# Kernel tuning notes

Hardware: AMD Instinct MI355X
Metric: run time of the kernel (lower is better)

The kernel has to match this reference:

```python
import jax, jax.numpy as jnp
import numpy as np

TAU = 1.0  # temperaturesa
GRID = 5   # torch.chunk(..., 5) along H and W


def _cam(X, gamma, tau):
    # Channel attention: energy = Xf Xf^T over spatial dim, with max-subtraction/negation trick.
    B, C, H, W = X.shape
    Xf = X.reshape(B, C, H * W)
    energy = jnp.einsum('bcn,bdn->bcd', Xf, Xf)                      # [B,C,C]
    energy_new = jnp.max(energy, axis=-1, keepdims=True) - energy
    attn = jax.nn.softmax(energy_new / tau, axis=-1)
    out = jnp.einsum('bcd,bdn->bcn', attn, Xf).reshape(B, C, H, W)
    return gamma * out + X


def _pam(X, Wq, bq, Wk, bk, Wv, bv, gamma, tau):
    # Position attention with 1x1-conv q/k/v (1x1 conv == channel matmul).
    B, C, H, W = X.shape
    N = H * W
    Xf = X.reshape(B, C, N)
    q = jnp.einsum('kc,bcn->bnk', Wq, Xf) + bq                        # [B,N,C//8]
    k = jnp.einsum('kc,bcn->bkn', Wk, Xf) + bk[None, :, None]         # [B,C//8,N]
    v = jnp.einsum('dc,bcn->bdn', Wv, Xf) + bv[None, :, None]         # [B,C,N]
    energy = jnp.einsum('bnk,bkm->bnm', q, k)                         # [B,N,N]
    attn = jax.nn.softmax(energy / tau, axis=-1)
    # torch: bmm(value, attention.permute(0,2,1)) -> out[b,d,m] = sum_n v[b,d,n]*attn[b,m,n]
    out = jnp.einsum('bdn,bmn->bdm', v, attn).reshape(B, C, H, W)
    return gamma * out + X


def _cka_loss(X, Y):
    # linear_CKA_loss: HKH centering done as K - rowmean - colmean + totalmean.
    def cgram(Z):
        K = Z @ Z.T                                                   # [B,B]
        rm = jnp.mean(K, axis=1, keepdims=True)
        cm = jnp.mean(K, axis=0, keepdims=True)
        return K - rm - cm + jnp.mean(K)
    cX, cY = cgram(X), cgram(Y)
    hsic = jnp.sum(cX * cY)
    v1 = jnp.sqrt(jnp.sum(cX * cX))
    v2 = jnp.sqrt(jnp.sum(cY * cY))
    return -jnp.log(jnp.abs(hsic / (v1 * v2)) + 1e-8)


def _grid_chunks(X, g=GRID):
    # 5x5 spatial tiling -> [g*g, B, C, H/g, W/g]
    B, C, H, W = X.shape
    h, w = H // g, W // g
    return X.reshape(B, C, g, h, g, w).transpose(2, 4, 0, 1, 3, 5).reshape(g * g, B, C, h, w)


def setup_inputs() -> dict:
    key = jax.random.key(0)
    ks = jax.random.split(key, 10)
    B, C, H, W = 16, 256, 80, 80
    Ck = C // 8
    return {
        'feat_S': jax.random.normal(ks[0], (B, C, H, W), jnp.float32),
        'feat_T': jax.random.normal(ks[1], (B, C, H, W), jnp.float32),
        'Wq': jax.random.normal(ks[2], (Ck, C), jnp.float32),
        'bq': jax.random.normal(ks[3], (Ck,), jnp.float32),
        'Wk': jax.random.normal(ks[4], (Ck, C), jnp.float32),
        'bk': jax.random.normal(ks[5], (Ck,), jnp.float32),
        'Wv': jax.random.normal(ks[6], (C, C), jnp.float32),
        'bv': jax.random.normal(ks[7], (C,), jnp.float32),
        'gammacam': jax.random.normal(ks[8], (1,), jnp.float32),
        'gammapam': jax.random.normal(ks[9], (1,), jnp.float32),
    }


def reference(feat_S, feat_T, Wq, bq, Wk, bk, Wv, bv, gammacam, gammapam):
    # feature_transform == 'separately_CAMgridPAM_CKA'
    tau = TAU
    pam = lambda X: _pam(X, Wq, bq, Wk, bk, Wv, bv, gammapam, tau)
    chunks_S = _grid_chunks(feat_S)                                   # [25,B,C,16,16]
    chunks_T = _grid_chunks(feat_T)
    pam_S = jax.vmap(pam)(chunks_S)
    pam_T = jax.vmap(pam)(chunks_T)
    nchunk, B = pam_S.shape[0], pam_S.shape[1]
    flat_S = pam_S.reshape(nchunk, B, -1)
    flat_T = pam_T.reshape(nchunk, B, -1)
    loss_PAM = jnp.mean(jax.vmap(_cka_loss)(flat_S, flat_T))          # sum/n == mean
    CAM_S = _cam(feat_S, gammacam, tau)
    CAM_T = _cam(feat_T, gammacam, tau)
    loss_CAM = _cka_loss(CAM_S.reshape(B, -1), CAM_T.reshape(B, -1))
    return (loss_CAM, loss_PAM)
```

## Files before the change

kernel.cpp:

```cpp
#include <hip/hip_runtime.h>


typedef short bf16x8 __attribute__((ext_vector_type(8)));
typedef float f32x4 __attribute__((ext_vector_type(4)));

constexpr int BB = 16;
constexpr int CH = 256;
constexpr int HW = 6400;
constexpr int IMW = 80;

__device__ __forceinline__ int lds_off(int row, int half, int k2) {
  return row * 128 + ((((half << 6)) | k2) ^ ((row & 7) << 4));
}

__device__ __forceinline__ bf16x8 frag_ld(const char* base, int row, int half, int lane) {
  int off = row * 128 + ((((half << 6)) | ((lane >> 4) << 4)) ^ ((lane & 7) << 4));
  return *(const bf16x8*)(base + off);
}

__device__ __forceinline__ void cvt2(float x, unsigned short& h, unsigned short& l) {
  unsigned u = __float_as_uint(x);
  h = (unsigned short)(u >> 16);
  float r = x - __uint_as_float(u & 0xffff0000u);
  l = (unsigned short)(__float_as_uint(r) >> 16);
}

__device__ __forceinline__ void cvt4(float4 v, ushort4& h, ushort4& l) {
  cvt2(v.x, h.x, l.x); cvt2(v.y, h.y, l.y);
  cvt2(v.z, h.z, l.z); cvt2(v.w, h.w, l.w);
}

__device__ __forceinline__ void cvt8(float4 v0, float4 v1, bf16x8& hi, bf16x8& lo) {
  unsigned short h, l;
  cvt2(v0.x, h, l); hi[0] = (short)h; lo[0] = (short)l;
  cvt2(v0.y, h, l); hi[1] = (short)h; lo[1] = (short)l;
  cvt2(v0.z, h, l); hi[2] = (short)h; lo[2] = (short)l;
  cvt2(v0.w, h, l); hi[3] = (short)h; lo[3] = (short)l;
  cvt2(v1.x, h, l); hi[4] = (short)h; lo[4] = (short)l;
  cvt2(v1.y, h, l); hi[5] = (short)h; lo[5] = (short)l;
  cvt2(v1.z, h, l); hi[6] = (short)h; lo[6] = (short)l;
  cvt2(v1.w, h, l); hi[7] = (short)h; lo[7] = (short)l;
}

__device__ __forceinline__ unsigned short bf_rnd(float x) {
  unsigned u = __float_as_uint(x);
  return (unsigned short)((u + 0x8000u) >> 16);
}

__global__ __launch_bounds__(512) void cam_energy_k(const float* __restrict__ fS,
                                                    const float* __restrict__ fT,
                                                    float* __restrict__ part) {
  const int kc = blockIdx.x, b = blockIdx.y, t = blockIdx.z;
  const float* X = (t ? fT : fS) + (size_t)b * CH * HW;
  __shared__ unsigned short lds[2 * 256 * 64];
  const int tid = threadIdx.x, lane = tid & 63, w = tid >> 6;
  const int wr = w >> 2, wc = w & 3;
  const int r0 = tid >> 1, half = tid & 1;
  const int kbase = kc * 800 + half * 32;
  const float* Xr = X + (size_t)r0 * HW + kbase;
  f32x4 acc[8][4] = {};
  float4 v[8];
#pragma unroll
  for (int q = 0; q < 8; ++q) v[q] = *(const float4*)(Xr + q * 4);
  for (int it = 0; it < 13; ++it) {
    char* pb = (char*)lds + (it & 1) * 32768;
#pragma unroll
    for (int q = 0; q < 8; ++q) {
      ushort4 u;
      u.x = bf_rnd(v[q].x); u.y = bf_rnd(v[q].y);
      u.z = bf_rnd(v[q].z); u.w = bf_rnd(v[q].w);
      *(ushort4*)(pb + lds_off(r0, half, q * 8)) = u;
    }
    __syncthreads();
    float4 nv[8];
    if (it < 12) {
      const int nk = (it + 1) * 64;
      if (nk + half * 32 < 800) {
        const float* Xn = Xr + nk;
#pragma unroll
        for (int q = 0; q < 8; ++q) nv[q] = *(const float4*)(Xn + q * 4);
      } else {
#pragma unroll
        for (int q = 0; q < 8; ++q) nv[q] = make_float4(0.f, 0.f, 0.f, 0.f);
      }
    }
    bf16x8 bfr[2][4];
#pragma unroll
    for (int h = 0; h < 2; ++h)
#pragma unroll
      for (int n = 0; n < 4; ++n)
        bfr[h][n] = frag_ld(pb, wc * 64 + n * 16 + (lane & 15), h, lane);
#pragma unroll
    for (int m = 0; m < 8; ++m) {
      int arow = wr * 128 + m * 16 + (lane & 15);
      bf16x8 a0 = frag_ld(pb, arow, 0, lane);
      bf16x8 a1 = frag_ld(pb, arow, 1, lane);
#pragma unroll
      for (int n = 0; n < 4; ++n)
        acc[m][n] = __builtin_amdgcn_mfma_f32_16x16x32_bf16(a0, bfr[0][n], acc[m][n], 0, 0, 0);
#pragma unroll
      for (int n = 0; n < 4; ++n)
        acc[m][n] = __builtin_amdgcn_mfma_f32_16x16x32_bf16(a1, bfr[1][n], acc[m][n], 0, 0, 0);
    }
#pragma unroll
    for (int q = 0; q < 8; ++q) v[q] = nv[q];
  }
  float* Eb = part + (((size_t)kc * 2 + t) * BB + b) * 65536;
#pragma unroll
  for (int m = 0; m < 8; ++m)
#pragma unroll
    for (int n = 0; n < 4; ++n) {
      int row = wr * 128 + m * 16 + ((lane >> 4) << 2);
      int col = wc * 64 + n * 16 + (lane & 15);
#pragma unroll
      for (int r2 = 0; r2 < 4; ++r2)
        Eb[(size_t)(row + r2) * 256 + col] = acc[m][n][r2];
    }
}

__global__ __launch_bounds__(64) void cam_softmax_k(float* __restrict__ part) {
  const int c = blockIdx.x, b = blockIdx.y, t = blockIdx.z;
  const size_t base = (((size_t)t * BB + b) * CH + c) * CH;
  const int lane = threadIdx.x;
  float4 x = make_float4(0.f, 0.f, 0.f, 0.f);
#pragma unroll
  for (int p = 0; p < 8; ++p) {
    float4 y = ((const float4*)(part + (size_t)p * 2097152 + base))[lane];
    x.x += y.x; x.y += y.y; x.z += y.z; x.w += y.w;
  }
  float mn = fminf(fminf(x.x, x.y), fminf(x.z, x.w));
  for (int o = 32; o; o >>= 1) mn = fminf(mn, __shfl_xor(mn, o));
  float4 p4;
  p4.x = __expf(mn - x.x); p4.y = __expf(mn - x.y);
  p4.z = __expf(mn - x.z); p4.w = __expf(mn - x.w);
  float s = (p4.x + p4.y) + (p4.z + p4.w);
  for (int o = 32; o; o >>= 1) s += __shfl_xor(s, o);
  const float inv = 1.0f / s;
  p4.x *= inv; p4.y *= inv; p4.z *= inv; p4.w *= inv;
  ((float4*)(part + base))[lane] = p4;
}

template <int MODE>
__global__ __launch_bounds__(512) void ax_k(const float* __restrict__ Abase, int Astride,
                                            const float* __restrict__ X,
                                            float* __restrict__ OUT,
                                            const float* __restrict__ bvec,
                                            const float* __restrict__ gsc) {
  const int nt = blockIdx.x;
  const int b = blockIdx.y;
  const float* A = Abase + (size_t)b * Astride;
  const float* Xb = X + (size_t)b * CH * HW;
  float* OUTb = OUT + (size_t)b * CH * HW;
  const int nbase = nt * 128;
  __shared__ unsigned short lds[(256 + 128) * 64];
  char* Ab = (char*)lds;
  char* Bb = (char*)lds + 32768;
  const int tid = threadIdx.x, lane = tid & 63, w = tid >> 6;
  const int wr = w >> 1, wc = w & 1;
  const int r0 = tid >> 1, kq = tid & 1;
  const int n4 = (tid & 31) * 4, c0l = tid >> 5;
  f32x4 acc[4][4] = {};
  float4 ra[4], rb[2];
#pragma unroll
  for (int q = 0; q < 4; ++q)
    ra[q] = *(const float4*)(A + (size_t)r0 * 256 + kq * 16 + q * 4);
#pragma unroll
  for (int q = 0; q < 2; ++q)
    rb[q] = *(const float4*)(Xb + (size_t)(c0l + 16 * q) * HW + nbase + n4);
  for (int s = 0; s < 8; ++s) {
#pragma unroll
    for (int q = 0; q < 4; ++q) {
      ushort4 h4, l4;
      cvt4(ra[q], h4, l4);
      *(ushort4*)(Ab + lds_off(r0, 0, kq * 32 + q * 8)) = h4;
      *(ushort4*)(Ab + lds_off(r0, 1, kq * 32 + q * 8)) = l4;
    }
#pragma unroll
    for (int q = 0; q < 2; ++q) {
      int cc = c0l + 16 * q;
      float4 v = rb[q];
#pragma unroll
      for (int jj = 0; jj < 4; ++jj) {
        int j = (jj + tid) & 3;
        float e = (j == 0) ? v.x : (j == 1) ? v.y : (j == 2) ? v.z : v.w;
        unsigned short h, l;
        cvt2(e, h, l);
        int row = n4 + j;
        *(unsigned short*)(Bb + lds_off(row, 0, cc * 2)) = h;
        *(unsigned short*)(Bb + lds_off(row, 1, cc * 2)) = l;
      }
    }
    __syncthreads();
    if (s < 7) {
      int k0 = (s + 1) * 32;
#pragma unroll
      for (int q = 0; q < 4; ++q)
        ra[q] = *(const float4*)(A + (size_t)r0 * 256 + k0 + kq * 16 + q * 4);
#pragma unroll
      for (int q = 0; q < 2; ++q)
        rb[q] = *(const float4*)(Xb + (size_t)(k0 + c0l + 16 * q) * HW + nbase + n4);
    }
    bf16x8 bfr[2][4];
#pragma unroll
    for (int h = 0; h < 2; ++h)
#pragma unroll
      for (int n = 0; n < 4; ++n)
        bfr[h][n] = frag_ld(Bb, wc * 64 + n * 16 + (lane & 15), h, lane);
#pragma unroll
    for (int m = 0; m < 4; ++m) {
      int arow = wr * 64 + m * 16 + (lane & 15);
      bf16x8 a0 = frag_ld(Ab, arow, 0, lane);
      bf16x8 a1 = frag_ld(Ab, arow, 1, lane);
#pragma unroll
      for (int n = 0; n < 4; ++n)
        acc[m][n] = __builtin_amdgcn_mfma_f32_16x16x32_bf16(a0, bfr[0][n], acc[m][n], 0, 0, 0);
#pragma unroll
      for (int n = 0; n < 4; ++n)
        acc[m][n] = __builtin_amdgcn_mfma_f32_16x16x32_bf16(a0, bfr[1][n], acc[m][n], 0, 0, 0);
#pragma unroll
      for (int n = 0; n < 4; ++n)
        acc[m][n] = __builtin_amdgcn_mfma_f32_16x16x32_bf16(a1, bfr[0][n], acc[m][n], 0, 0, 0);
    }
    __syncthreads();
  }
  float g = 0.f;
  if (MODE == 0) g = gsc[0];
#pragma unroll
  for (int m = 0; m < 4; ++m)
#pragma unroll
    for (int n = 0; n < 4; ++n) {
      int row = wr * 64 + m * 16 + ((lane >> 4) << 2);
      int col = nbase + wc * 64 + n * 16 + (lane & 15);
#pragma unroll
      for (int r2 = 0; r2 < 4; ++r2) {
        size_t o = (size_t)(row + r2) * HW + col;
        float v = acc[m][n][r2];
        if (MODE == 0) OUTb[o] = g * v + Xb[o];
        else           OUTb[o] = v + bvec[row + r2];
      }
    }
}

__global__ __launch_bounds__(256) void qk_k(const float* __restrict__ X,
                                            const float* __restrict__ Wq,
                                            const float* __restrict__ bq,
                                            const float* __restrict__ Wk,
                                            const float* __restrict__ bk,
                                            float* __restrict__ qt,
                                            float* __restrict__ kf) {
  const int nbase = blockIdx.x * 256;
  const int b = blockIdx.y;
  const float* Xb = X + (size_t)b * CH * HW;
  __shared__ unsigned short lds[(64 + 256) * 64];
  char* Ab = (char*)lds;
  char* Bb = (char*)lds + 8192;
  const int tid = threadIdx.x, lane = tid & 63, w = tid >> 6;
  const int ar = tid >> 2, akq = tid & 3;
  const int n4 = (tid & 63) * 4, c0l = tid >> 6;
  const float* Arow = (ar < 32) ? (Wq + (size_t)ar * CH) : (Wk + (size_t)(ar - 32) * CH);
  f32x4 acc[4][4] = {};
  float4 va[2], vb[8];
#pragma unroll
  for (int q = 0; q < 2; ++q)
    va[q] = *(const float4*)(Arow + akq * 8 + q * 4);
#pragma unroll
  for (int q = 0; q < 8; ++q)
    vb[q] = *(const float4*)(Xb + (size_t)(c0l + 4 * q) * HW + nbase + n4);
  for (int s = 0; s < 8; ++s) {
    __syncthreads();
#pragma unroll
    for (int q = 0; q < 2; ++q) {
      ushort4 h4, l4;
      cvt4(va[q], h4, l4);
      *(ushort4*)(Ab + lds_off(ar, 0, akq * 16 + q * 8)) = h4;
      *(ushort4*)(Ab + lds_off(ar, 1, akq * 16 + q * 8)) = l4;
    }
#pragma unroll
    for (int q = 0; q < 8; ++q) {
      int cc = c0l + 4 * q;
      float4 v = vb[q];
#pragma unroll
      for (int jj = 0; jj < 4; ++jj) {
        int j = (jj + tid) & 3;
        float e = (j == 0) ? v.x : (j == 1) ? v.y : (j == 2) ? v.z : v.w;
        unsigned short h, l;
        cvt2(e, h, l);
        int row = n4 + j;
        *(unsigned short*)(Bb + lds_off(row, 0, cc * 2)) = h;
        *(unsigned short*)(Bb + lds_off(row, 1, cc * 2)) = l;
      }
    }
    __syncthreads();
    float4 na[2], nb[8];
    if (s < 7) {
      const int k0 = (s + 1) * 32;
#pragma unroll
      for (int q = 0; q < 2; ++q)
        na[q] = *(const float4*)(Arow + k0 + akq * 8 + q * 4);
#pragma unroll
      for (int q = 0; q < 8; ++q)
        nb[q] = *(const float4*)(Xb + (size_t)(k0 + c0l + 4 * q) * HW + nbase + n4);
    }
    bf16x8 bfr[2][4];
#pragma unroll
    for (int h = 0; h < 2; ++h)
#pragma unroll
      for (int n = 0; n < 4; ++n)
        bfr[h][n] = frag_ld(Bb, w * 64 + n * 16 + (lane & 15), h, lane);
#pragma unroll
    for (int m = 0; m < 4; ++m) {
      int arow2 = m * 16 + (lane & 15);
      bf16x8 a0 = frag_ld(Ab, arow2, 0, lane);
      bf16x8 a1 = frag_ld(Ab, arow2, 1, lane);
#pragma unroll
      for (int n = 0; n < 4; ++n)
        acc[m][n] = __builtin_amdgcn_mfma_f32_16x16x32_bf16(a0, bfr[0][n], acc[m][n], 0, 0, 0);
#pragma unroll
      for (int n = 0; n < 4; ++n)
        acc[m][n] = __builtin_amdgcn_mfma_f32_16x16x32_bf16(a0, bfr[1][n], acc[m][n], 0, 0, 0);
#pragma unroll
      for (int n = 0; n < 4; ++n)
        acc[m][n] = __builtin_amdgcn_mfma_f32_16x16x32_bf16(a1, bfr[0][n], acc[m][n], 0, 0, 0);
    }
#pragma unroll
    for (int q = 0; q < 2; ++q) va[q] = na[q];
#pragma unroll
    for (int q = 0; q < 8; ++q) vb[q] = nb[q];
  }
#pragma unroll
  for (int m = 0; m < 4; ++m)
#pragma unroll
    for (int n = 0; n < 4; ++n) {
      int row = m * 16 + ((lane >> 4) << 2);
      int col = nbase + w * 64 + n * 16 + (lane & 15);
#pragma unroll
      for (int r2 = 0; r2 < 4; ++r2) {
        int rr = row + r2;
        float v = acc[m][n][r2];
        if (rr < 32) qt[((size_t)b * HW + col) * 32 + rr] = v + bq[rr];
        else         kf[((size_t)b * 32 + (rr - 32)) * HW + col] = v + bk[rr - 32];
      }
    }
}

__global__ __launch_bounds__(256) void pam_es_k(const float* __restrict__ qt,
                                                const float* __restrict__ kf,
                                                float* __restrict__ Pbuf) {
  const int ccb = blockIdx.x;
  const int ck = ccb >> 4, b = ccb & 15;
  const int gi = ck / 5, gj = ck % 5;
  const int pbase = gi * 16 * IMW + gj * 16;
  float* Pc = Pbuf + (size_t)ccb * 65536;
  __shared__ float qs[256][32];
  __shared__ float S[32][256];
  const int tid = threadIdx.x;
  const float* qb = qt + (size_t)b * HW * 32;
#pragma unroll
  for (int qq = 0; qq < 8; ++qq) {
    int j = (tid >> 3) + 32 * qq;
    int nj = pbase + (j >> 4) * IMW + (j & 15);
    float4 v = *(const float4*)(qb + (size_t)nj * 32 + (tid & 7) * 4);
    *(float4*)&qs[j][(tid & 7) * 4] = v;
  }
  const int nt = pbase + (tid >> 4) * IMW + (tid & 15);
  const float* kb = kf + (size_t)b * 32 * HW;
  float kc[32];
#pragma unroll
  for (int kk = 0; kk < 32; ++kk) kc[kk] = kb[(size_t)kk * HW + nt];
  __syncthreads();
  const int w = tid >> 6, lane = tid & 63;
  for (int p = 0; p < 8; ++p) {
#pragma unroll 4
    for (int j2 = 0; j2 < 32; ++j2) {
      int row = p * 32 + j2;
      float s = 0.f;
#pragma unroll
      for (int k8 = 0; k8 < 8; ++k8) {
        float4 qv = *(const float4*)&qs[row][k8 * 4];
        s = fmaf(qv.x, kc[k8 * 4 + 0], s);
        s = fmaf(qv.y, kc[k8 * 4 + 1], s);
        s = fmaf(qv.z, kc[k8 * 4 + 2], s);
        s = fmaf(qv.w, kc[k8 * 4 + 3], s);
      }
      S[j2][tid] = s;
    }
    __syncthreads();
#pragma unroll
    for (int rr = 0; rr < 8; ++rr) {
      int jj = w * 8 + rr;
      float4 v = *(const float4*)&S[jj][lane << 2];
      float m = fmaxf(fmaxf(v.x, v.y), fmaxf(v.z, v.w));
      for (int o = 32; o; o >>= 1) m = fmaxf(m, __shfl_xor(m, o));
      float4 pv;
      pv.x = __expf(v.x - m); pv.y = __expf(v.y - m);
      pv.z = __expf(v.z - m); pv.w = __expf(v.w - m);
      float s = (pv.x + pv.y) + (pv.z + pv.w);
      for (int o = 32; o; o >>= 1) s += __shfl_xor(s, o);
      const float inv = 1.f / s;
      pv.x *= inv; pv.y *= inv; pv.z *= inv; pv.w *= inv;
      *(float4*)&Pc[(size_t)(p * 32 + jj) * 256 + (lane << 2)] = pv;
    }
    __syncthreads();
  }
}

__global__ __launch_bounds__(512) void pam_pv_k(float* __restrict__ P,
                                                const float* __restrict__ V,
                                                const float* __restrict__ fS,
                                                const float* __restrict__ fT,
                                                const float* __restrict__ gsc, int t) {
  const int ccb = blockIdx.x;
  const int ck = ccb >> 4, b = ccb & 15;
  const int gi = ck / 5, gj = ck % 5;
  const float* Xb = (t ? fT : fS) + (size_t)b * CH * HW;
  const float* Vb = V + (size_t)b * CH * HW;
  float* Pc = P + (size_t)ccb * 65536;
  __shared__ unsigned short lds[2 * 256 * 64];
  char* Ab = (char*)lds;
  char* Bb = (char*)lds + 32768;
  const int tid = threadIdx.x, lane = tid & 63, w = tid >> 6;
  const int wr = w >> 2, wc = w & 3;
  const int r0 = tid >> 3, kq = tid & 7;
  const int pbase = gi * 16 * IMW + gj * 16;
  f32x4 acc[8][4] = {};
  float4 va[4], vb[4];
  {
    int jj = kq * 4;
    int ngl = pbase + (jj >> 4) * IMW + (jj & 15);
#pragma unroll
    for (int q = 0; q < 4; ++q) {
      int rr = r0 + 64 * q;
      va[q] = *(const float4*)(Vb + (size_t)rr * HW + ngl);
      vb[q] = *(const float4*)(Pc + (size_t)rr * 256 + kq * 4);
    }
  }
  for (int s = 0; s < 8; ++s) {
    __syncthreads();
#pragma unroll
    for (int q = 0; q < 4; ++q) {
      int rr = r0 + 64 * q;
      ushort4 h4, l4;
      cvt4(va[q], h4, l4);
      *(ushort4*)(Ab + lds_off(rr, 0, kq * 8)) = h4;
      *(ushort4*)(Ab + lds_off(rr, 1, kq * 8)) = l4;
      cvt4(vb[q], h4, l4);
      *(ushort4*)(Bb + lds_off(rr, 0, kq * 8)) = h4;
      *(ushort4*)(Bb + lds_off(rr, 1, kq * 8)) = l4;
    }
    __syncthreads();
    float4 na[4], nb[4];
    if (s < 7) {
      int k0 = (s + 1) * 32;
      int jj = k0 + kq * 4;
      int ngl = pbase + (jj >> 4) * IMW + (jj & 15);
#pragma unroll
      for (int q = 0; q < 4; ++q) {
        int rr = r0 + 64 * q;
        na[q] = *(const float4*)(Vb + (size_t)rr * HW + ngl);
        nb[q] = *(const float4*)(Pc + (size_t)rr * 256 + k0 + kq * 4);
      }
    }
    bf16x8 bfr[2][4];
#pragma unroll
    for (int h = 0; h < 2; ++h)
#pragma unroll
      for (int n = 0; n < 4; ++n)
        bfr[h][n] = frag_ld(Bb, wc * 64 + n * 16 + (lane & 15), h, lane);
#pragma unroll
    for (int m = 0; m < 8; ++m) {
      int arow = wr * 128 + m * 16 + (lane & 15);
      bf16x8 a0 = frag_ld(Ab, arow, 0, lane);
      bf16x8 a1 = frag_ld(Ab, arow, 1, lane);
#pragma unroll
      for (int n = 0; n < 4; ++n)
        acc[m][n] = __builtin_amdgcn_mfma_f32_16x16x32_bf16(a0, bfr[0][n], acc[m][n], 0, 0, 0);
#pragma unroll
      for (int n = 0; n < 4; ++n)
        acc[m][n] = __builtin_amdgcn_mfma_f32_16x16x32_bf16(a0, bfr[1][n], acc[m][n], 0, 0, 0);
#pragma unroll
      for (int n = 0; n < 4; ++n)
        acc[m][n] = __builtin_amdgcn_mfma_f32_16x16x32_bf16(a1, bfr[0][n], acc[m][n], 0, 0, 0);
    }
#pragma unroll
    for (int q = 0; q < 4; ++q) { va[q] = na[q]; vb[q] = nb[q]; }
  }
  const float g = gsc[0];
#pragma unroll
  for (int m = 0; m < 8; ++m)
#pragma unroll
    for (int n = 0; n < 4; ++n) {
      int row = wr * 128 + m * 16 + ((lane >> 4) << 2);
      int col = wc * 64 + n * 16 + (lane & 15);
      int ngl = pbase + (col >> 4) * IMW + (col & 15);
#pragma unroll
      for (int r2 = 0; r2 < 4; ++r2) {
        float v = g * acc[m][n][r2] + Xb[(size_t)(row + r2) * HW + ngl];
        Pc[(size_t)(row + r2) * 256 + col] = v;
      }
    }
}

__global__ __launch_bounds__(256) void gram_mfma_k(const float* __restrict__ Z,
                                                   size_t gStride, size_t bStride,
                                                   double* __restrict__ G) {
  const int tid = threadIdx.x, lane = tid & 63, w = tid >> 6;
  const float* Zg = Z + (size_t)blockIdx.y * gStride;
  const float* p = Zg + (size_t)(lane & 15) * bStride +
                   (size_t)blockIdx.x * 4096 + w * 1024 + ((lane >> 4) << 3);
  f32x4 acc = {};
#pragma unroll 4
  for (int s = 0; s < 32; ++s) {
    float4 v0 = *(const float4*)(p + s * 32);
    float4 v1 = *(const float4*)(p + s * 32 + 4);
    bf16x8 hi, lo;
    cvt8(v0, v1, hi, lo);
    acc = __builtin_amdgcn_mfma_f32_16x16x32_bf16(hi, hi, acc, 0, 0, 0);
    acc = __builtin_amdgcn_mfma_f32_16x16x32_bf16(hi, lo, acc, 0, 0, 0);
    acc = __builtin_amdgcn_mfma_f32_16x16x32_bf16(lo, hi, acc, 0, 0, 0);
  }
  double* Gt = G + (size_t)blockIdx.y * 256;
  const int col = lane & 15, row0 = (lane >> 4) << 2;
#pragma unroll
  for (int i = 0; i < 4; ++i)
    atomicAdd(&Gt[(size_t)(row0 + i) * 16 + col], (double)acc[i]);
}

__global__ __launch_bounds__(256) void cka_pair_k(const double* __restrict__ G,
                                                  double* __restrict__ losses) {
  const int q = blockIdx.x;
  const double* KX = (q == 0) ? G : G + 512 + (size_t)(q - 1) * 256;
  const double* KY = (q == 0) ? G + 256 : G + 512 + 6400 + (size_t)(q - 1) * 256;
  __shared__ double red[256];
  __shared__ double srm[16], scm[16];
  __shared__ double stm;
  const int tid = threadIdx.x;
  const int r = tid >> 4, c = tid & 15;

  auto center = [&](double k) -> double {
    red[tid] = k;
    __syncthreads();
    for (int off = 8; off; off >>= 1) {
      if (c < off) red[tid] += red[tid + off];
      __syncthreads();
    }
    if (c == 0) srm[r] = red[tid] * (1.0 / 16.0);
    __syncthreads();
    red[c * 16 + r] = k;
    __syncthreads();
    for (int off = 8; off; off >>= 1) {
      if (r < off) red[c * 16 + r] += red[c * 16 + r + off];
      __syncthreads();
    }
    if (r == 0) scm[c] = red[c * 16] * (1.0 / 16.0);
    __syncthreads();
    if (tid == 0) {
      double s = 0.0;
      for (int i = 0; i < 16; ++i) s += srm[i];
      stm = s * (1.0 / 16.0);
    }
    __syncthreads();
    double v = k - srm[r] - scm[c] + stm;
    __syncthreads();
    return v;
  };
  auto reduce_sum = [&](double v) -> double {
    red[tid] = v;
    __syncthreads();
    for (int off = 128; off; off >>= 1) {
      if (tid < off) red[tid] += red[tid + off];
      __syncthreads();
    }
    double s = red[0];
    __syncthreads();
    return s;
  };
  double cx = center(KX[tid]);
  double cy = center(KY[tid]);
  double h = reduce_sum(cx * cy);
  double v1 = reduce_sum(cx * cx);
  double v2 = reduce_sum(cy * cy);
  if (tid == 0) losses[q] = -log(fabs(h / (sqrt(v1) * sqrt(v2))) + 1e-8);
}

__global__ void cka_combine_k(const double* __restrict__ losses,
                              float* __restrict__ out) {
  if (threadIdx.x == 0) {
    out[0] = (float)losses[0];
    double s = 0.0;
    for (int q = 1; q <= 25; ++q) s += losses[q];
    out[1] = (float)(s * (1.0 / 25.0));
  }
}

extern "C" void kernel_launch(void* const* d_in, const int* in_sizes, int n_in,
                              void* d_out, int out_size, void* d_ws, size_t ws_size,
                              hipStream_t stream) {
  (void)in_sizes; (void)n_in; (void)out_size; (void)ws_size;
  const float* fS = (const float*)d_in[0];
  const float* fT = (const float*)d_in[1];
  const float* Wq = (const float*)d_in[2];
  const float* bq = (const float*)d_in[3];
  const float* Wk = (const float*)d_in[4];
  const float* bk = (const float*)d_in[5];
  const float* Wv = (const float*)d_in[6];
  const float* bv = (const float*)d_in[7];
  const float* gcam = (const float*)d_in[8];
  const float* gpam = (const float*)d_in[9];
  float* out = (float*)d_out;

  float* buf0 = (float*)d_ws;
  float* buf1 = buf0 + 26214400;
  double* G = (double*)(buf1 + 26214400);
  float* Pbuf = buf1;
  float* qt = buf0;
  float* kf = buf0 + 3276800;
  double* losses = (double*)buf0;

  hipMemsetAsync(G, 0, 13312 * sizeof(double), stream);

  cam_energy_k<<<dim3(8, 16, 2), 512, 0, stream>>>(fS, fT, buf1);
  cam_softmax_k<<<dim3(256, 16, 2), 64, 0, stream>>>(buf1);
  for (int t = 0; t < 2; ++t) {
    ax_k<0><<<dim3(50, 16), 512, 0, stream>>>(buf1 + (size_t)t * BB * 65536, 65536,
                                              t ? fT : fS, buf0, nullptr, gcam);
    gram_mfma_k<<<dim3(400, 1), 256, 0, stream>>>(buf0, (size_t)0, (size_t)1638400,
                                                  G + t * 256);
  }
  for (int t = 0; t < 2; ++t) {
    const float* X = t ? fT : fS;
    qk_k<<<dim3(25, 16), 256, 0, stream>>>(X, Wq, bq, Wk, bk, qt, kf);
    pam_es_k<<<dim3(400), 256, 0, stream>>>(qt, kf, Pbuf);
    ax_k<1><<<dim3(50, 16), 512, 0, stream>>>(Wv, 0, X, buf0, bv, nullptr);
    pam_pv_k<<<dim3(400), 512, 0, stream>>>(Pbuf, buf0, fS, fT, gpam, t);
    gram_mfma_k<<<dim3(16, 25), 256, 0, stream>>>(Pbuf, (size_t)1048576, (size_t)65536,
                                                  G + 512 + t * 6400);
  }
  cka_pair_k<<<dim3(26), 256, 0, stream>>>(G, losses);
  cka_combine_k<<<dim3(1), 64, 0, stream>>>(losses, out);
}
```

Before: 1.072 ms.

## Use 1024-thread blocks for CAM energy and AX GEMMs, double-buffer AX LDS

Doubles the block size of cam_energy_k and ax_k to 1024 threads (16 waves), halving the per-wave accumulator tiles so each wave holds fewer registers and more waves hide latency. ax_k now double-buffers its LDS tiles, which removes the trailing barrier per k-step. Its B-tile loads become per-column scalar loads packed into ushort4 stores instead of scattered 2-byte stores. The risk is more fragment reloads from LDS per MFMA, higher LDS usage (96KB in ax_k) limiting blocks per CU, and uncoalesced-looking scalar global loads.

```diff
diff --git a/kernel.cpp b/kernel.cpp
--- a/kernel.cpp
+++ b/kernel.cpp
@@ -47,70 +47,66 @@
   return (unsigned short)((u + 0x8000u) >> 16);
 }
 
-__global__ __launch_bounds__(512) void cam_energy_k(const float* __restrict__ fS,
-                                                    const float* __restrict__ fT,
-                                                    float* __restrict__ part) {
+__global__ __launch_bounds__(1024) void cam_energy_k(const float* __restrict__ fS,
+                                                     const float* __restrict__ fT,
+                                                     float* __restrict__ part) {
   const int kc = blockIdx.x, b = blockIdx.y, t = blockIdx.z;
   const float* X = (t ? fT : fS) + (size_t)b * CH * HW;
   __shared__ unsigned short lds[2 * 256 * 64];
   const int tid = threadIdx.x, lane = tid & 63, w = tid >> 6;
   const int wr = w >> 2, wc = w & 3;
-  const int r0 = tid >> 1, half = tid & 1;
-  const int kbase = kc * 800 + half * 32;
-  const float* Xr = X + (size_t)r0 * HW + kbase;
-  f32x4 acc[8][4] = {};
-  float4 v[8];
-#pragma unroll
-  for (int q = 0; q < 8; ++q) v[q] = *(const float4*)(Xr + q * 4);
+  const int r0 = tid >> 2, kq = tid & 3;
+  const int half = kq >> 1, k2b = (kq & 1) * 32;
+  const float* Xr = X + (size_t)r0 * HW + kc * 800 + kq * 16;
+  f32x4 acc[4][4] = {};
+  float4 v[4];
+#pragma unroll
+  for (int q = 0; q < 4; ++q) v[q] = *(const float4*)(Xr + q * 4);
   for (int it = 0; it < 13; ++it) {
     char* pb = (char*)lds + (it & 1) * 32768;
 #pragma unroll
-    for (int q = 0; q < 8; ++q) {
+    for (int q = 0; q < 4; ++q) {
       ushort4 u;
       u.x = bf_rnd(v[q].x); u.y = bf_rnd(v[q].y);
       u.z = bf_rnd(v[q].z); u.w = bf_rnd(v[q].w);
-      *(ushort4*)(pb + lds_off(r0, half, q * 8)) = u;
-    }
-    __syncthreads();
-    float4 nv[8];
+      *(ushort4*)(pb + lds_off(r0, half, k2b + q * 8)) = u;
+    }
+    __syncthreads();
+    float4 nv[4];
     if (it < 12) {
       const int nk = (it + 1) * 64;
-      if (nk + half * 32 < 800) {
+      if (nk + kq * 16 < 800) {
         const float* Xn = Xr + nk;
 #pragma unroll
-        for (int q = 0; q < 8; ++q) nv[q] = *(const float4*)(Xn + q * 4);
+        for (int q = 0; q < 4; ++q) nv[q] = *(const float4*)(Xn + q * 4);
       } else {
 #pragma unroll
-        for (int q = 0; q < 8; ++q) nv[q] = make_float4(0.f, 0.f, 0.f, 0.f);
-      }
-    }
-    bf16x8 bfr[2][4];
-#pragma unroll
-    for (int h = 0; h < 2; ++h)
-#pragma unroll
-      for (int n = 0; n < 4; ++n)
-        bfr[h][n] = frag_ld(pb, wc * 64 + n * 16 + (lane & 15), h, lane);
-#pragma unroll
-    for (int m = 0; m < 8; ++m) {
-      int arow = wr * 128 + m * 16 + (lane & 15);
-      bf16x8 a0 = frag_ld(pb, arow, 0, lane);
-      bf16x8 a1 = frag_ld(pb, arow, 1, lane);
-#pragma unroll
-      for (int n = 0; n < 4; ++n)
-        acc[m][n] = __builtin_amdgcn_mfma_f32_16x16x32_bf16(a0, bfr[0][n], acc[m][n], 0, 0, 0);
-#pragma unroll
-      for (int n = 0; n < 4; ++n)
-        acc[m][n] = __builtin_amdgcn_mfma_f32_16x16x32_bf16(a1, bfr[1][n], acc[m][n], 0, 0, 0);
-    }
-#pragma unroll
-    for (int q = 0; q < 8; ++q) v[q] = nv[q];
+        for (int q = 0; q < 4; ++q) nv[q] = make_float4(0.f, 0.f, 0.f, 0.f);
+      }
+    }
+#pragma unroll
+    for (int h = 0; h < 2; ++h) {
+      bf16x8 bh[4];
+#pragma unroll
+      for (int n = 0; n < 4; ++n)
+        bh[n] = frag_ld(pb, wc * 64 + n * 16 + (lane & 15), h, lane);
+#pragma unroll
+      for (int m = 0; m < 4; ++m) {
+        bf16x8 a = frag_ld(pb, wr * 64 + m * 16 + (lane & 15), h, lane);
+#pragma unroll
+        for (int n = 0; n < 4; ++n)
+          acc[m][n] = __builtin_amdgcn_mfma_f32_16x16x32_bf16(a, bh[n], acc[m][n], 0, 0, 0);
+      }
+    }
+#pragma unroll
+    for (int q = 0; q < 4; ++q) v[q] = nv[q];
   }
   float* Eb = part + (((size_t)kc * 2 + t) * BB + b) * 65536;
 #pragma unroll
-  for (int m = 0; m < 8; ++m)
+  for (int m = 0; m < 4; ++m)
 #pragma unroll
     for (int n = 0; n < 4; ++n) {
-      int row = wr * 128 + m * 16 + ((lane >> 4) << 2);
+      int row = wr * 64 + m * 16 + ((lane >> 4) << 2);
       int col = wc * 64 + n * 16 + (lane & 15);
 #pragma unroll
       for (int r2 = 0; r2 < 4; ++r2)
@@ -141,96 +137,89 @@
 }
 
 template <int MODE>
-__global__ __launch_bounds__(512) void ax_k(const float* __restrict__ Abase, int Astride,
-                                            const float* __restrict__ X,
-                                            float* __restrict__ OUT,
-                                            const float* __restrict__ bvec,
-                                            const float* __restrict__ gsc) {
+__global__ __launch_bounds__(1024) void ax_k(const float* __restrict__ Abase, int Astride,
+                                             const float* __restrict__ X,
+                                             float* __restrict__ OUT,
+                                             const float* __restrict__ bvec,
+                                             const float* __restrict__ gsc) {
   const int nt = blockIdx.x;
   const int b = blockIdx.y;
   const float* A = Abase + (size_t)b * Astride;
   const float* Xb = X + (size_t)b * CH * HW;
   float* OUTb = OUT + (size_t)b * CH * HW;
   const int nbase = nt * 128;
-  __shared__ unsigned short lds[(256 + 128) * 64];
-  char* Ab = (char*)lds;
-  char* Bb = (char*)lds + 32768;
+  __shared__ unsigned short lds[2 * (256 + 128) * 64];
   const int tid = threadIdx.x, lane = tid & 63, w = tid >> 6;
-  const int wr = w >> 1, wc = w & 1;
-  const int r0 = tid >> 1, kq = tid & 1;
-  const int n4 = (tid & 31) * 4, c0l = tid >> 5;
-  f32x4 acc[4][4] = {};
-  float4 ra[4], rb[2];
-#pragma unroll
-  for (int q = 0; q < 4; ++q)
-    ra[q] = *(const float4*)(A + (size_t)r0 * 256 + kq * 16 + q * 4);
+  const int wr = w >> 2, wc = w & 3;
+  const int r0 = tid >> 2, kq = tid & 3;
+  const int n_r = tid & 127, kg = tid >> 7;
+  const float* Xcol = Xb + nbase + n_r;
+  f32x4 acc[4][2] = {};
+  float4 ra[2];
+  float vb4[4];
 #pragma unroll
   for (int q = 0; q < 2; ++q)
-    rb[q] = *(const float4*)(Xb + (size_t)(c0l + 16 * q) * HW + nbase + n4);
+    ra[q] = *(const float4*)(A + (size_t)r0 * 256 + kq * 8 + q * 4);
+#pragma unroll
+  for (int e = 0; e < 4; ++e)
+    vb4[e] = Xcol[(size_t)(kg * 4 + e) * HW];
   for (int s = 0; s < 8; ++s) {
-#pragma unroll
-    for (int q = 0; q < 4; ++q) {
+    char* Ab = (char*)lds + (s & 1) * 49152;
+    char* Bb = Ab + 32768;
+#pragma unroll
+    for (int q = 0; q < 2; ++q) {
       ushort4 h4, l4;
       cvt4(ra[q], h4, l4);
-      *(ushort4*)(Ab + lds_off(r0, 0, kq * 32 + q * 8)) = h4;
-      *(ushort4*)(Ab + lds_off(r0, 1, kq * 32 + q * 8)) = l4;
-    }
-#pragma unroll
-    for (int q = 0; q < 2; ++q) {
-      int cc = c0l + 16 * q;
-      float4 v = rb[q];
-#pragma unroll
-      for (int jj = 0; jj < 4; ++jj) {
-        int j = (jj + tid) & 3;
-        float e = (j == 0) ? v.x : (j == 1) ? v.y : (j == 2) ? v.z : v.w;
-        unsigned short h, l;
-        cvt2(e, h, l);
-        int row = n4 + j;
-        *(unsigned short*)(Bb + lds_off(row, 0, cc * 2)) = h;
-        *(unsigned short*)(Bb + lds_off(row, 1, cc * 2)) = l;
-      }
+      *(ushort4*)(Ab + lds_off(r0, 0, kq * 16 + q * 8)) = h4;
+      *(ushort4*)(Ab + lds_off(r0, 1, kq * 16 + q * 8)) = l4;
+    }
+    {
+      unsigned short bh[4], bl[4];
+#pragma unroll
+      for (int e = 0; e < 4; ++e) cvt2(vb4[e], bh[e], bl[e]);
+      *(ushort4*)(Bb + lds_off(n_r, 0, kg * 8)) = make_ushort4(bh[0], bh[1], bh[2], bh[3]);
+      *(ushort4*)(Bb + lds_off(n_r, 1, kg * 8)) = make_ushort4(bl[0], bl[1], bl[2], bl[3]);
     }
     __syncthreads();
     if (s < 7) {
       int k0 = (s + 1) * 32;
 #pragma unroll
-      for (int q = 0; q < 4; ++q)
-        ra[q] = *(const float4*)(A + (size_t)r0 * 256 + k0 + kq * 16 + q * 4);
-#pragma unroll
       for (int q = 0; q < 2; ++q)
-        rb[q] = *(const float4*)(Xb + (size_t)(k0 + c0l + 16 * q) * HW + nbase + n4);
-    }
-    bf16x8 bfr[2][4];
+        ra[q] = *(const float4*)(A + (size_t)r0 * 256 + k0 + kq * 8 + q * 4);
+#pragma unroll
+      for (int e = 0; e < 4; ++e)
+        vb4[e] = Xcol[(size_t)(k0 + kg * 4 + e) * HW];
+    }
+    bf16x8 bfr[2][2];
 #pragma unroll
     for (int h = 0; h < 2; ++h)
 #pragma unroll
-      for (int n = 0; n < 4; ++n)
-        bfr[h][n] = frag_ld(Bb, wc * 64 + n * 16 + (lane & 15), h, lane);
+      for (int n = 0; n < 2; ++n)
+        bfr[h][n] = frag_ld(Bb, wc * 32 + n * 16 + (lane & 15), h, lane);
 #pragma unroll
     for (int m = 0; m < 4; ++m) {
       int arow = wr * 64 + m * 16 + (lane & 15);
       bf16x8 a0 = frag_ld(Ab, arow, 0, lane);
       bf16x8 a1 = frag_ld(Ab, arow, 1, lane);
 #pragma unroll
-      for (int n = 0; n < 4; ++n)
+      for (int n = 0; n < 2; ++n)
         acc[m][n] = __builtin_amdgcn_mfma_f32_16x16x32_bf16(a0, bfr[0][n], acc[m][n], 0, 0, 0);
 #pragma unroll
-      for (int n = 0; n < 4; ++n)
+      for (int n = 0; n < 2; ++n)
         acc[m][n] = __builtin_amdgcn_mfma_f32_16x16x32_bf16(a0, bfr[1][n], acc[m][n], 0, 0, 0);
 #pragma unroll
-      for (int n = 0; n < 4; ++n)
+      for (int n = 0; n < 2; ++n)
         acc[m][n] = __builtin_amdgcn_mfma_f32_16x16x32_bf16(a1, bfr[0][n], acc[m][n], 0, 0, 0);
     }
-    __syncthreads();
   }
   float g = 0.f;
   if (MODE == 0) g = gsc[0];
 #pragma unroll
   for (int m = 0; m < 4; ++m)
 #pragma unroll
-    for (int n = 0; n < 4; ++n) {
+    for (int n = 0; n < 2; ++n) {
       int row = wr * 64 + m * 16 + ((lane >> 4) << 2);
-      int col = nbase + wc * 64 + n * 16 + (lane & 15);
+      int col = nbase + wc * 32 + n * 16 + (lane & 15);
 #pragma unroll
       for (int r2 = 0; r2 < 4; ++r2) {
         size_t o = (size_t)(row + r2) * HW + col;
@@ -618,11 +607,11 @@
 
   hipMemsetAsync(G, 0, 13312 * sizeof(double), stream);
 
-  cam_energy_k<<<dim3(8, 16, 2), 512, 0, stream>>>(fS, fT, buf1);
+  cam_energy_k<<<dim3(8, 16, 2), 1024, 0, stream>>>(fS, fT, buf1);
   cam_softmax_k<<<dim3(256, 16, 2), 64, 0, stream>>>(buf1);
   for (int t = 0; t < 2; ++t) {
-    ax_k<0><<<dim3(50, 16), 512, 0, stream>>>(buf1 + (size_t)t * BB * 65536, 65536,
-                                              t ? fT : fS, buf0, nullptr, gcam);
+    ax_k<0><<<dim3(50, 16), 1024, 0, stream>>>(buf1 + (size_t)t * BB * 65536, 65536,
+                                               t ? fT : fS, buf0, nullptr, gcam);
     gram_mfma_k<<<dim3(400, 1), 256, 0, stream>>>(buf0, (size_t)0, (size_t)1638400,
                                                   G + t * 256);
   }
@@ -630,7 +619,7 @@
     const float* X = t ? fT : fS;
     qk_k<<<dim3(25, 16), 256, 0, stream>>>(X, Wq, bq, Wk, bk, qt, kf);
     pam_es_k<<<dim3(400), 256, 0, stream>>>(qt, kf, Pbuf);
-    ax_k<1><<<dim3(50, 16), 512, 0, stream>>>(Wv, 0, X, buf0, bv, nullptr);
+    ax_k<1><<<dim3(50, 16), 1024, 0, stream>>>(Wv, 0, X, buf0, bv, nullptr);
     pam_pv_k<<<dim3(400), 512, 0, stream>>>(Pbuf, buf0, fS, fT, gpam, t);
     gram_mfma_k<<<dim3(16, 25), 256, 0, stream>>>(Pbuf, (size_t)1048576, (size_t)65536,
                                                   G + 512 + t * 6400);
```

Result: faster. 1.001 ms (-6.6%).
